# Kernel tuning notes

Measured on AMD Instinct MI355X. Metric: run time of the kernel, lower is better.

The kernel has to match this reference:

```python
import jax, jax.numpy as jnp
import numpy as np

ACT_BIT = 8
WEIGHT_BIT = 8
GELU_K = 1.4142
GELU_CONST = 14
C0, C1 = -0.2888, -1.769
C2 = 1.0 / C0  # coeff[2] /= coeff[0]


def round_ste(x):
    return x + jax.lax.stop_gradient(jnp.round(x) - x)


def floor_ste(x):
    return x + jax.lax.stop_gradient(jnp.floor(x) - x)


def sym_scale(bit, smin, smax):
    # symmetric_linear_quantization_params
    n = 2 ** (bit - 1) - 1
    return jnp.clip(jnp.maximum(jnp.abs(smin), jnp.abs(smax)), 1e-8, None) / n


def quant_linear(x, sf_in, weight, bias):
    # per-channel symmetric int8 weight quant, int32 bias, scaled int GEMM
    n = 2 ** (WEIGHT_BIT - 1) - 1
    w_sf = sym_scale(WEIGHT_BIT, weight.min(axis=1), weight.max(axis=1))  # [O]
    w_int = jnp.clip(round_ste(weight / w_sf[:, None]), -n - 1, n)       # [O,H]
    bias_sf = w_sf * sf_in                                               # [O]
    b_int = round_ste(bias / bias_sf)
    x_int = x / sf_in                                                    # [B,S,H]
    out_int = jnp.einsum('bsh,oh->bso', x_int, w_int) + b_int
    return out_int * bias_sf, bias_sf


def int_gelu(x, sf):
    # integer polynomial erf approximation (I-BERT IntGELU)
    x_int = x / sf
    sf_e = sf / GELU_K
    b_int = jnp.floor(C1 / sf_e)
    c_int = jnp.floor(C2 / sf_e ** 2)
    sign = jnp.sign(x_int)
    abs_int = jnp.minimum(jnp.abs(x_int), -b_int)
    y_int = sign * ((abs_int + b_int) ** 2 + c_int)
    sf_sig = sf_e ** 2 * C0
    y_int = floor_ste(y_int / 2.0 ** GELU_CONST)
    sf_sig = sf_sig * 2 ** GELU_CONST
    shift_int = jnp.floor(1.0 / sf_sig)
    x_int = x_int * (y_int + shift_int)
    sf_out = sf * sf_sig / 2
    return x_int * sf_out, sf_out


def quant_act(x, pre_sf):
    # QuantAct: requantize to 8 bits via dyadic (frexp) fixed-point multiply
    n = 2 ** (ACT_BIT - 1) - 1
    sf = sym_scale(ACT_BIT, x.min(), x.max())  # scalar
    z_int = jnp.round(x / pre_sf)
    m, e = jnp.frexp(pre_sf / sf)              # pre_sf is per-channel [O]
    m_int = jnp.round(m * 2.0 ** 31)
    out_int = jnp.clip(jnp.round(z_int * m_int / 2.0 ** (31 - e)), -n - 1, n)
    # FixedPointMul backward is identity w.r.t. x (straight-through)
    q_int = x + jax.lax.stop_gradient(out_int - x)
    return q_int * sf, sf


def setup_inputs() -> dict:
    key = jax.random.key(0)
    k1, k2, k3 = jax.random.split(key, 3)
    B, S, H, I = 8, 2048, 1024, 4096
    sf = jnp.array([0.02], dtype=jnp.float32)
    x = jax.random.normal(k1, (B, S, H), dtype=jnp.float32)
    # pre-quantized 8-bit activations on the incoming grid
    x = jnp.clip(jnp.round(x / sf) * sf, -128 * 0.02, 127 * 0.02)
    weight = jax.random.normal(k2, (I, H), dtype=jnp.float32) * 0.02
    bias = jax.random.normal(k3, (I,), dtype=jnp.float32) * 0.01
    return {"hidden_states": x, "hidden_states_scaling_factor": sf,
            "weight": weight, "bias": bias}


def reference(hidden_states, hidden_states_scaling_factor, weight, bias):
    h, sf = quant_linear(hidden_states, hidden_states_scaling_factor, weight, bias)
    h, sf = int_gelu(h, sf)
    h, sf = quant_act(h, sf)
    return h, sf
```

## Files before the change

### kernel.cpp

```cpp
#include <hip/hip_runtime.h>

#define M_TOK 16384
#define K_DIM 1024
#define N_DIM 4096
#define SLABA ((size_t)M_TOK * 64)
#define SLABB ((size_t)N_DIM * 64)

using i32x4 = __attribute__((ext_vector_type(4))) int;
using f32x4 = __attribute__((ext_vector_type(4))) float;

__device__ __forceinline__ void gld16(char* lds, const char* g) {
  __builtin_amdgcn_global_load_lds(
      (const __attribute__((address_space(1))) void*)g,
      (__attribute__((address_space(3))) void*)lds, 16, 0, 0);
}

__device__ __forceinline__ float gelu_q(int acc, float4 pa, float4 pb) {
  float xi = (float)acc + pa.x;
  float sgn = (xi > 0.f) ? 1.f : ((xi < 0.f) ? -1.f : 0.f);
  float ab  = fminf(fabsf(xi), -pa.z);
  float tt  = ab + pa.z;
  float yi  = sgn * (tt * tt + pa.w);
  yi = floorf(yi * (1.0f / 16384.0f));
  return xi * (yi + pb.x);
}

__global__ void k_prep_x(const float* __restrict__ x,
                         const float* __restrict__ sfp,
                         char* __restrict__ x8) {
  float r = 1.0f / sfp[0];
  int i4 = blockIdx.x * 256 + threadIdx.x;
  f32x4 v = __builtin_nontemporal_load((const f32x4*)x + i4);
  int c0 = (int)rintf(v.x * r);
  int c1 = (int)rintf(v.y * r);
  int c2 = (int)rintf(v.z * r);
  int c3 = (int)rintf(v.w * r);
  int packed = (c0 & 0xFF) | ((c1 & 0xFF) << 8) | ((c2 & 0xFF) << 16)
             | ((c3 & 0xFF) << 24);
  int m = i4 >> 8, kq = i4 & 255;
  ((int*)(x8 + (size_t)(kq >> 4) * SLABA + (size_t)m * 64))[kq & 15] = packed;
}

__global__ void k_prep_w(const float* __restrict__ W,
                         const float* __restrict__ bias,
                         const float* __restrict__ sfp,
                         char* __restrict__ w8,
                         float4* __restrict__ cA,
                         float4* __restrict__ cB) {
  const int o = blockIdx.x;
  const int t = threadIdx.x;
  float4 wv = ((const float4*)(W + (size_t)o * K_DIM))[t];
  float vmn = fminf(fminf(wv.x, wv.y), fminf(wv.z, wv.w));
  float vmx = fmaxf(fmaxf(wv.x, wv.y), fmaxf(wv.z, wv.w));
#pragma unroll
  for (int off = 32; off; off >>= 1) {
    vmn = fminf(vmn, __shfl_down(vmn, off, 64));
    vmx = fmaxf(vmx, __shfl_down(vmx, off, 64));
  }
  __shared__ float sm[8];
  __shared__ float s_wsf;
  int lane = t & 63, wv_id = t >> 6;
  if (lane == 0) { sm[wv_id] = vmn; sm[4 + wv_id] = vmx; }
  __syncthreads();
  if (t == 0) {
    float mn = fminf(fminf(sm[0], sm[1]), fminf(sm[2], sm[3]));
    float mx = fmaxf(fmaxf(sm[4], sm[5]), fmaxf(sm[6], sm[7]));
    float wsf = fmaxf(fmaxf(fabsf(mn), fabsf(mx)), 1e-8f) / 127.0f;
    s_wsf = wsf;
    float sfin = sfp[0];
    float bsf  = wsf * sfin;
    float bint = rintf(bias[o] / bsf);
    float sfe  = bsf / 1.4142f;
    float bg   = floorf(-1.769f / sfe);
    const float C2F = (float)(1.0 / -0.2888);
    float cg   = floorf(C2F / (sfe * sfe));
    float sfsig = sfe * sfe * (-0.2888f);
    sfsig = sfsig * 16384.0f;
    float shiftint = floorf(1.0f / sfsig);
    float sfout = bsf * sfsig / 2.0f;
    cA[o] = make_float4(bint, bsf, bg, cg);
    cB[o] = make_float4(shiftint, sfout, 0.0f, 0.0f);
  }
  __syncthreads();
  float wsf = s_wsf;
  int q0 = (int)fminf(fmaxf(rintf(wv.x / wsf), -128.f), 127.f);
  int q1 = (int)fminf(fmaxf(rintf(wv.y / wsf), -128.f), 127.f);
  int q2 = (int)fminf(fmaxf(rintf(wv.z / wsf), -128.f), 127.f);
  int q3 = (int)fminf(fmaxf(rintf(wv.w / wsf), -128.f), 127.f);
  int packed = (q0 & 0xFF) | ((q1 & 0xFF) << 8) | ((q2 & 0xFF) << 16)
             | ((q3 & 0xFF) << 24);
  ((int*)(w8 + (size_t)(t >> 4) * SLABB + (size_t)o * 64))[t & 15] = packed;
}

__global__ __launch_bounds__(256) void k_gemm(
    const char* __restrict__ A, const char* __restrict__ B,
    const float4* __restrict__ cA, const float4* __restrict__ cB,
    float* __restrict__ out, float2* __restrict__ pmm) {
  const int t = threadIdx.x;
  const int lane = t & 63;
  const int w = t >> 6;
  const int wm = w >> 1, wn = w & 1;

  const int lin = blockIdx.y * gridDim.x + blockIdx.x;
  const int xcd = lin & 7;
  const int local = lin >> 3;
  const int bx = xcd * 4 + (local & 3);
  const int by = local >> 2;
  const int m0 = by * 128;
  const int n0 = bx * 128;

  const int fr = lane & 15;
  const int hi16 = (lane >> 4) * 16;

  __shared__ char Ab[2][8192];
  __shared__ char Bb[2][8192];

  int aoff[4], boff[4];
#pragma unroll
  for (int i = 0; i < 4; ++i) {
    aoff[i] = (wm * 64 + i * 16 + fr) * 64 + hi16;
    boff[i] = (wn * 64 + i * 16 + fr) * 64 + hi16;
  }

  const char* Abase = A + (size_t)m0 * 64;
  const char* Bbase = B + (size_t)n0 * 64;
  const int c0 = w * 1024 + lane * 16;
  const int c1 = (w + 4) * 1024 + lane * 16;
  const int l0 = w * 1024, l1 = (w + 4) * 1024;

  {
    const char* As = Abase;
    const char* Bs = Bbase;
    gld16(&Ab[0][l0], As + c0);
    gld16(&Ab[0][l1], As + c1);
    gld16(&Bb[0][l0], Bs + c0);
    gld16(&Bb[0][l1], Bs + c1);
  }
  __syncthreads();

  i32x4 acc[4][4] = {};
  for (int it = 0; it < K_DIM / 64; ++it) {
    const int cur = it & 1;
    if (it + 1 < K_DIM / 64) {
      const char* As = Abase + (size_t)(it + 1) * SLABA;
      const char* Bs = Bbase + (size_t)(it + 1) * SLABB;
      gld16(&Ab[cur ^ 1][l0], As + c0);
      gld16(&Ab[cur ^ 1][l1], As + c1);
      gld16(&Bb[cur ^ 1][l0], Bs + c0);
      gld16(&Bb[cur ^ 1][l1], Bs + c1);
    }
    i32x4 af[4], bf[4];
#pragma unroll
    for (int i = 0; i < 4; ++i) {
      af[i] = *(const i32x4*)(&Ab[cur][aoff[i]]);
      bf[i] = *(const i32x4*)(&Bb[cur][boff[i]]);
    }
#pragma unroll
    for (int mi = 0; mi < 4; ++mi)
#pragma unroll
      for (int ni = 0; ni < 4; ++ni)
        acc[mi][ni] = __builtin_amdgcn_mfma_i32_16x16x64_i8(
            af[mi], bf[ni], acc[mi][ni], 0, 0, 0);
    __syncthreads();
  }

  const int rowb = m0 + wm * 64 + (lane >> 4) * 4;
  const int colb = n0 + wn * 64 + fr;
  float vmin = 3.4e38f, vmax = -3.4e38f;

#pragma unroll
  for (int ni = 0; ni < 4; ++ni) {
    const int col = colb + ni * 16;
    const float4 pa = cA[col];
    const float4 pb = cB[col];
    float qmn = 3.4e38f, qmx = -3.4e38f;
#pragma unroll
    for (int mi = 0; mi < 4; ++mi) {
#pragma unroll
      for (int r = 0; r < 4; ++r) {
        float q = gelu_q(acc[mi][ni][r], pa, pb);
        qmn = fminf(qmn, q);
        qmx = fmaxf(qmx, q);
        __builtin_nontemporal_store(
            q, &out[(size_t)(rowb + mi * 16 + r) * N_DIM + col]);
      }
    }
    float xa = qmn * pb.y, xb = qmx * pb.y;
    vmin = fminf(vmin, fminf(xa, xb));
    vmax = fmaxf(vmax, fmaxf(xa, xb));
  }

#pragma unroll
  for (int off = 32; off; off >>= 1) {
    vmin = fminf(vmin, __shfl_down(vmin, off, 64));
    vmax = fmaxf(vmax, __shfl_down(vmax, off, 64));
  }
  __shared__ float swmn[4], swmx[4];
  if (lane == 0) { swmn[w] = vmin; swmx[w] = vmax; }
  __syncthreads();
  if (t == 0) {
    float bmn = fminf(fminf(swmn[0], swmn[1]), fminf(swmn[2], swmn[3]));
    float bmx = fmaxf(fmaxf(swmx[0], swmx[1]), fmaxf(swmx[2], swmx[3]));
    pmm[lin] = make_float2(bmn, bmx);
  }
}

__global__ void k_scalar(const float2* __restrict__ pmm,
                         const float4* __restrict__ cB,
                         float* __restrict__ cR,
                         float* __restrict__ sfws,
                         float* __restrict__ out_sf) {
  const int t = threadIdx.x;
  float mn = 3.4e38f, mx = -3.4e38f;
  for (int i = t; i < 4096; i += 256) {
    float2 p = pmm[i];
    mn = fminf(mn, p.x);
    mx = fmaxf(mx, p.y);
  }
#pragma unroll
  for (int off = 32; off; off >>= 1) {
    mn = fminf(mn, __shfl_down(mn, off, 64));
    mx = fmaxf(mx, __shfl_down(mx, off, 64));
  }
  __shared__ float sm[8];
  __shared__ float s_sf;
  int lane = t & 63, wid = t >> 6;
  if (lane == 0) { sm[wid] = mn; sm[4 + wid] = mx; }
  __syncthreads();
  if (t == 0) {
    float m0 = fminf(fminf(sm[0], sm[1]), fminf(sm[2], sm[3]));
    float m1 = fmaxf(fmaxf(sm[4], sm[5]), fmaxf(sm[6], sm[7]));
    float sf = fmaxf(fmaxf(fabsf(m0), fabsf(m1)), 1e-8f) / 127.0f;
    s_sf = sf;
    if (blockIdx.x == 0) { sfws[0] = sf; out_sf[0] = sf; }
  }
  __syncthreads();
  float sf = s_sf;
  int o = blockIdx.x * 256 + t;
  float psf = cB[o].y;
  int e;
  float mm = frexpf(psf / sf, &e);
  float mi = rintf(mm * 2147483648.0f);
  cR[o] = mi * ldexpf(1.0f, e - 31);
}

__global__ __launch_bounds__(256) void k_requant(
    float* __restrict__ out, const float* __restrict__ cR,
    const float* __restrict__ sfws) {
  const float sf = sfws[0];
  const size_t n4 = (size_t)M_TOK * N_DIM / 4;
  for (size_t i4 = (size_t)blockIdx.x * 256 + threadIdx.x; i4 < n4;
       i4 += (size_t)gridDim.x * 256) {
    f32x4 v = __builtin_nontemporal_load((const f32x4*)out + i4);
    int col4 = (int)(i4 & (N_DIM / 4 - 1));
    float4 c = ((const float4*)cR)[col4];
    v.x = fminf(fmaxf(rintf(rintf(v.x) * c.x), -128.f), 127.f) * sf;
    v.y = fminf(fmaxf(rintf(rintf(v.y) * c.y), -128.f), 127.f) * sf;
    v.z = fminf(fmaxf(rintf(rintf(v.z) * c.z), -128.f), 127.f) * sf;
    v.w = fminf(fmaxf(rintf(rintf(v.w) * c.w), -128.f), 127.f) * sf;
    __builtin_nontemporal_store(v, (f32x4*)out + i4);
  }
}

extern "C" void kernel_launch(void* const* d_in, const int* in_sizes, int n_in,
                              void* d_out, int out_size, void* d_ws, size_t ws_size,
                              hipStream_t stream) {
  const float* x    = (const float*)d_in[0];
  const float* sfp  = (const float*)d_in[1];
  const float* W    = (const float*)d_in[2];
  const float* bias = (const float*)d_in[3];
  float* out = (float*)d_out;

  char* ws = (char*)d_ws;
  char* x8 = ws;
  char* w8 = ws + (size_t)M_TOK * K_DIM;
  char* tail = ws + (size_t)M_TOK * K_DIM + (size_t)N_DIM * K_DIM;
  float4* cA = (float4*)tail;
  float4* cB = (float4*)(tail + (size_t)N_DIM * 16);
  float* cR  = (float*)(tail + (size_t)N_DIM * 32);
  float2* pmm = (float2*)(tail + (size_t)N_DIM * 36);
  float* sfws = (float*)(tail + (size_t)N_DIM * 36 + 32768);

  k_prep_x<<<(M_TOK * K_DIM / 4) / 256, 256, 0, stream>>>(x, sfp, x8);
  k_prep_w<<<N_DIM, 256, 0, stream>>>(W, bias, sfp, w8, cA, cB);
  k_gemm<<<dim3(N_DIM / 128, M_TOK / 128), 256, 0, stream>>>(
      x8, w8, cA, cB, out, pmm);
  k_scalar<<<N_DIM / 256, 256, 0, stream>>>(pmm, cB, cR, sfws,
                                            out + (size_t)M_TOK * N_DIM);
  k_requant<<<8192, 256, 0, stream>>>(out, cR, sfws);
}
```

Baseline: 488.3 us.

## Triple-buffer int8 GEMM LDS tiles with XOR swizzle and one barrier per step

```diff
diff --git a/kernel.cpp b/kernel.cpp
--- a/kernel.cpp
+++ b/kernel.cpp
@@ -112,42 +112,49 @@
   const int fr = lane & 15;
   const int hi16 = (lane >> 4) * 16;
 
-  __shared__ char Ab[2][8192];
-  __shared__ char Bb[2][8192];
-
+  __shared__ char Ab[3][8192];
+  __shared__ char Bb[3][8192];
+
+  const int rsw = ((fr >> 1) & 3) << 4;
   int aoff[4], boff[4];
 #pragma unroll
   for (int i = 0; i < 4; ++i) {
-    aoff[i] = (wm * 64 + i * 16 + fr) * 64 + hi16;
-    boff[i] = (wn * 64 + i * 16 + fr) * 64 + hi16;
+    aoff[i] = (wm * 64 + i * 16 + fr) * 64 + (hi16 ^ rsw);
+    boff[i] = (wn * 64 + i * 16 + fr) * 64 + (hi16 ^ rsw);
   }
 
   const char* Abase = A + (size_t)m0 * 64;
   const char* Bbase = B + (size_t)n0 * 64;
-  const int c0 = w * 1024 + lane * 16;
-  const int c1 = (w + 4) * 1024 + lane * 16;
+  const int srow = (lane >> 2);
+  const int schunk = ((lane & 3) ^ ((lane >> 3) & 3)) << 4;
+  const int c0 = (w * 16 + srow) * 64 + schunk;
+  const int c1 = (w * 16 + 64 + srow) * 64 + schunk;
   const int l0 = w * 1024, l1 = (w + 4) * 1024;
 
-  {
-    const char* As = Abase;
-    const char* Bs = Bbase;
-    gld16(&Ab[0][l0], As + c0);
-    gld16(&Ab[0][l1], As + c1);
-    gld16(&Bb[0][l0], Bs + c0);
-    gld16(&Bb[0][l1], Bs + c1);
-  }
-  __syncthreads();
+  gld16(&Ab[0][l0], Abase + c0);
+  gld16(&Ab[0][l1], Abase + c1);
+  gld16(&Bb[0][l0], Bbase + c0);
+  gld16(&Bb[0][l1], Bbase + c1);
+  gld16(&Ab[1][l0], Abase + SLABA + c0);
+  gld16(&Ab[1][l1], Abase + SLABA + c1);
+  gld16(&Bb[1][l0], Bbase + SLABB + c0);
+  gld16(&Bb[1][l1], Bbase + SLABB + c1);
 
   i32x4 acc[4][4] = {};
-  for (int it = 0; it < K_DIM / 64; ++it) {
-    const int cur = it & 1;
-    if (it + 1 < K_DIM / 64) {
-      const char* As = Abase + (size_t)(it + 1) * SLABA;
-      const char* Bs = Bbase + (size_t)(it + 1) * SLABB;
-      gld16(&Ab[cur ^ 1][l0], As + c0);
-      gld16(&Ab[cur ^ 1][l1], As + c1);
-      gld16(&Bb[cur ^ 1][l0], Bs + c0);
-      gld16(&Bb[cur ^ 1][l1], Bs + c1);
+#pragma unroll 3
+  for (int it = 0; it < 15; ++it) {
+    const int cur = it % 3;
+    const int nxt = (it + 2) % 3;
+    asm volatile("s_waitcnt vmcnt(4)" ::: "memory");
+    __builtin_amdgcn_s_barrier();
+    __builtin_amdgcn_sched_barrier(0);
+    if (it < 14) {
+      const char* As = Abase + (size_t)(it + 2) * SLABA;
+      const char* Bs = Bbase + (size_t)(it + 2) * SLABB;
+      gld16(&Ab[nxt][l0], As + c0);
+      gld16(&Ab[nxt][l1], As + c1);
+      gld16(&Bb[nxt][l0], Bs + c0);
+      gld16(&Bb[nxt][l1], Bs + c1);
     }
     i32x4 af[4], bf[4];
 #pragma unroll
@@ -161,7 +168,23 @@
       for (int ni = 0; ni < 4; ++ni)
         acc[mi][ni] = __builtin_amdgcn_mfma_i32_16x16x64_i8(
             af[mi], bf[ni], acc[mi][ni], 0, 0, 0);
-    __syncthreads();
+  }
+  {
+    asm volatile("s_waitcnt vmcnt(0)" ::: "memory");
+    __builtin_amdgcn_s_barrier();
+    __builtin_amdgcn_sched_barrier(0);
+    i32x4 af[4], bf[4];
+#pragma unroll
+    for (int i = 0; i < 4; ++i) {
+      af[i] = *(const i32x4*)(&Ab[0][aoff[i]]);
+      bf[i] = *(const i32x4*)(&Bb[0][boff[i]]);
+    }
+#pragma unroll
+    for (int mi = 0; mi < 4; ++mi)
+#pragma unroll
+      for (int ni = 0; ni < 4; ++ni)
+        acc[mi][ni] = __builtin_amdgcn_mfma_i32_16x16x64_i8(
+            af[mi], bf[ni], acc[mi][ni], 0, 0, 0);
   }
 
   const int rowb = m0 + wm * 64 + (lane >> 4) * 4;
```

Result: slower. 509.0 us (+4.2%).
